# Optimization experiments

Hardware: AMD Instinct MI355X
Metric: run time of the kernel (lower is better)

The kernel has to match this reference:

```python
import jax, jax.numpy as jnp
import numpy as np
import math

B, L, H, E, D = 4, 1024, 8, 64, 64
T_STEPS = 1000


def setup_inputs() -> dict:
    key = jax.random.key(0)
    ks = jax.random.split(key, 6)
    queries = jax.random.normal(ks[0], (B, L, H, E), dtype=jnp.float32)
    keys = jax.random.normal(ks[1], (B, L, H, E), dtype=jnp.float32)
    values = jax.random.normal(ks[2], (B, L, H, D), dtype=jnp.float32)
    sigma = jax.random.normal(ks[3], (B, L, H), dtype=jnp.float32)
    sqrt_alphas_cumprod = jax.random.uniform(ks[4], (T_STEPS,), dtype=jnp.float32)
    t = jax.random.randint(ks[5], (B,), 0, T_STEPS)
    return {
        "queries": queries,
        "keys": keys,
        "values": values,
        "sigma": sigma,
        "sqrt_alphas_cumprod": sqrt_alphas_cumprod,
        "t": t,
    }


def reference(queries, keys, values, sigma, sqrt_alphas_cumprod, t):
    B_, L_, H_, E_ = queries.shape
    scale = 1.0 / math.sqrt(E_)

    # scores: [B,H,L,S]
    scores = jnp.einsum("blhe,bshe->bhls", queries, keys)
    # causal mask (triu, diagonal=1) -> -inf, then scale (mask_flag=True, attn_mask=None)
    causal = jnp.triu(jnp.ones((L_, L_), dtype=bool), k=1)
    attn = scale * jnp.where(causal, -jnp.inf, scores)

    # sigma pipeline: [B,L,H] -> [B,H,L] -> nonlinear chain
    sg = jnp.transpose(sigma, (0, 2, 1))               # [B,H,L]
    sg = jax.nn.sigmoid(sg * 5.0) + 1e-5
    sg = jnp.power(3.0, sg) - 1.0                      # in (0, 2)

    # per-batch diffusion scale: sqrt_alphas_cumprod[t] -> [B,1,1]
    sac_t = sqrt_alphas_cumprod[t][:, None, None]      # [B,1,1]
    sigma_t = jnp.broadcast_to((sac_t * sg)[..., None], (B_, H_, L_, L_))

    # |i-j| distance matrix, Gaussian prior
    idx = jnp.arange(L_)
    dist = jnp.abs(idx[:, None] - idx[None, :]).astype(jnp.float32)  # [L,L]
    inv_sqrt_2pi = 1.0 / math.sqrt(2.0 * math.pi)
    prior = inv_sqrt_2pi / sigma_t * jnp.exp(-(dist ** 2) / 2.0 / (sigma_t ** 2))

    series = jax.nn.softmax(attn, axis=-1)             # dropout p=0.0
    V = jnp.einsum("bhls,bshd->blhd", series, values)
    return V, series, prior, sigma_t
```

## Files before the change

### kernel.cpp

```cpp
#include <hip/hip_runtime.h>
#include <hip/hip_bf16.h>
#include <cstddef>
#include <cstdint>

namespace {

using f32x4  = __attribute__((ext_vector_type(4))) float;
using bf16x8 = __attribute__((ext_vector_type(8))) short;
using u16x2  = __attribute__((ext_vector_type(2))) unsigned short;
using u16x4  = __attribute__((ext_vector_type(4))) unsigned short;

constexpr int TOTAL_BLOCKS = 9216;
constexpr int PSTR = 1032;

__device__ inline unsigned short f2bf(float x) {
  __hip_bfloat16 hv = __float2bfloat16(x);
  return *reinterpret_cast<unsigned short*>(&hv);
}
__device__ inline float bf2f(unsigned short u) {
  return __uint_as_float(((unsigned int)u) << 16);
}
__device__ inline bf16x8 pack_bf8(f32x4 a, f32x4 b) {
  bf16x8 r;
  r[0] = (short)f2bf(a[0]); r[1] = (short)f2bf(a[1]);
  r[2] = (short)f2bf(a[2]); r[3] = (short)f2bf(a[3]);
  r[4] = (short)f2bf(b[0]); r[5] = (short)f2bf(b[1]);
  r[6] = (short)f2bf(b[2]); r[7] = (short)f2bf(b[3]);
  return r;
}

__global__ __launch_bounds__(256) void fused_all(
    const float* __restrict__ Qg, const float* __restrict__ Kg,
    const float* __restrict__ Vg, const float* __restrict__ Sg,
    const float* __restrict__ sacg, const int* __restrict__ tg,
    float* __restrict__ outV, float* __restrict__ outS,
    float* __restrict__ outP, float* __restrict__ outT)
{
  __shared__ unsigned short Pl[32 * PSTR];
  __shared__ unsigned short Vt[64 * 72];
  __shared__ float red[4][32];
  __shared__ float invl[32];

  const int tid = threadIdx.x;
  const int bid = blockIdx.x;
  const int role9 = bid / 9;

  if (bid - role9 * 9 != 0) {
    const int pb = role9 * 8 + (bid - role9 * 9) - 1;
    const int r0 = pb * 4 + (tid >> 6);
    const int ln = tid & 63;
    const int b  = r0 >> 13;
    const int hh = (r0 >> 10) & 7;
    const int l  = r0 & 1023;
    const float sgv = Sg[(size_t)(b * 1024 + l) * 8 + hh];
    const float sac = sacg[tg[b]];
    const float sig = 1.f / (1.f + __expf(-5.f * sgv)) + 1e-5f;
    const float st  = sac * expm1f(sig * 1.0986122886681098f);
    const float coef = 0.3989422804014327f / st;
    const float qc   = -0.5f / (st * st);
    float* pp = outP + ((size_t)r0 << 10);
    float* tp = outT + ((size_t)r0 << 10);
    const f32x4 stv = {st, st, st, st};
#pragma unroll
    for (int j = 0; j < 4; ++j) {
      const int c0 = j * 256 + ln * 4;
      const float d0 = (float)(l - c0);
      const float d1 = d0 - 1.f, d2 = d0 - 2.f, d3 = d0 - 3.f;
      f32x4 pr;
      pr[0] = coef * __expf(qc * d0 * d0);
      pr[1] = coef * __expf(qc * d1 * d1);
      pr[2] = coef * __expf(qc * d2 * d2);
      pr[3] = coef * __expf(qc * d3 * d3);
      __builtin_nontemporal_store(pr, reinterpret_cast<f32x4*>(pp + c0));
      __builtin_nontemporal_store(stv, reinterpret_cast<f32x4*>(tp + c0));
    }
    return;
  }

  const int aid = role9;
  const int w = tid >> 6, ln = tid & 63;
  const int g = ln >> 4, n16 = ln & 15;
  const int bh = aid & 31, b = bh >> 3, h = bh & 7;
  const int qt = 31 - (aid >> 5);
  const int qb = qt * 32;
  const int nch = (qt >> 1) + 1;

  const float* Qbase = Qg + ((size_t)(b * 1024) * 8 + h) * 64;
  const float* Kbase = Kg + ((size_t)(b * 1024) * 8 + h) * 64;
  const float* Vbase = Vg + ((size_t)(b * 1024) * 8 + h) * 64;

  bf16x8 qf[2][2];
#pragma unroll
  for (int u = 0; u < 2; ++u) {
    const float* qr = Qbase + (size_t)(qb + u * 16 + n16) * 512 + 8 * g;
    qf[u][0] = pack_bf8(*(const f32x4*)(qr),      *(const f32x4*)(qr + 4));
    qf[u][1] = pack_bf8(*(const f32x4*)(qr + 32), *(const f32x4*)(qr + 36));
  }

  f32x4 O[2] = {};
  float cs[2] = {0.f, 0.f};

  const int spair = tid & 31, dgrp = tid >> 5;

  for (int c = 0; c < nch; ++c) {
    const float* kr = Kbase + (size_t)(c * 64 + w * 16 + n16) * 512 + 8 * g;
    const bf16x8 kf0 = pack_bf8(*(const f32x4*)(kr),      *(const f32x4*)(kr + 4));
    const bf16x8 kf1 = pack_bf8(*(const f32x4*)(kr + 32), *(const f32x4*)(kr + 36));

    const float* vb = Vbase + (size_t)(c * 64 + 2 * spair) * 512 + dgrp * 8;
    const f32x4 va0 = *(const f32x4*)(vb);
    const f32x4 va1 = *(const f32x4*)(vb + 4);
    const f32x4 vc0 = *(const f32x4*)(vb + 512);
    const f32x4 vc1 = *(const f32x4*)(vb + 516);

    __syncthreads();

#pragma unroll
    for (int i = 0; i < 4; ++i) {
      u16x2 w0 = {f2bf(va0[i]), f2bf(vc0[i])};
      *reinterpret_cast<u16x2*>(&Vt[(dgrp * 8 + i) * 72 + 2 * spair]) = w0;
      u16x2 w1 = {f2bf(va1[i]), f2bf(vc1[i])};
      *reinterpret_cast<u16x2*>(&Vt[(dgrp * 8 + 4 + i) * 72 + 2 * spair]) = w1;
    }

#pragma unroll
    for (int u = 0; u < 2; ++u) {
      f32x4 acc = {0.f, 0.f, 0.f, 0.f};
      acc = __builtin_amdgcn_mfma_f32_16x16x32_bf16(kf0, qf[u][0], acc, 0, 0, 0);
      acc = __builtin_amdgcn_mfma_f32_16x16x32_bf16(kf1, qf[u][1], acc, 0, 0, 0);
      const int qlane = qb + u * 16 + n16;
      const int sbase = c * 64 + w * 16 + 4 * g;
      const float e0 = (sbase + 0 <= qlane) ? __expf(acc[0] * 0.125f) : 0.f;
      const float e1 = (sbase + 1 <= qlane) ? __expf(acc[1] * 0.125f) : 0.f;
      const float e2 = (sbase + 2 <= qlane) ? __expf(acc[2] * 0.125f) : 0.f;
      const float e3 = (sbase + 3 <= qlane) ? __expf(acc[3] * 0.125f) : 0.f;
      cs[u] += (e0 + e1) + (e2 + e3);
      u16x4 pk = {f2bf(e0), f2bf(e1), f2bf(e2), f2bf(e3)};
      *reinterpret_cast<u16x4*>(&Pl[(u * 16 + n16) * PSTR + sbase]) = pk;
    }

    __syncthreads();

#pragma unroll
    for (int u = 0; u < 2; ++u)
#pragma unroll
      for (int h2 = 0; h2 < 2; ++h2) {
        const bf16x8 pa =
            *reinterpret_cast<const bf16x8*>(&Pl[(u * 16 + n16) * PSTR + c * 64 + h2 * 32 + 8 * g]);
        const bf16x8 vv =
            *reinterpret_cast<const bf16x8*>(&Vt[(w * 16 + n16) * 72 + h2 * 32 + 8 * g]);
        O[u] = __builtin_amdgcn_mfma_f32_16x16x32_bf16(pa, vv, O[u], 0, 0, 0);
      }
  }

  cs[0] += __shfl_xor(cs[0], 16); cs[0] += __shfl_xor(cs[0], 32);
  cs[1] += __shfl_xor(cs[1], 16); cs[1] += __shfl_xor(cs[1], 32);
  if (ln < 16) { red[w][n16] = cs[0]; red[w][16 + n16] = cs[1]; }
  __syncthreads();
  if (tid < 32) {
    const float s = red[0][tid] + red[1][tid] + red[2][tid] + red[3][tid];
    invl[tid] = 1.f / s;
  }
  __syncthreads();

  {
    float* Vo = outV + ((size_t)(b * 1024) * 8 + h) * 64;
#pragma unroll
    for (int u = 0; u < 2; ++u)
#pragma unroll
      for (int r = 0; r < 4; ++r) {
        const int qrow = u * 16 + 4 * g + r;
        __builtin_nontemporal_store(O[u][r] * invl[qrow],
                                    Vo + (size_t)(qb + qrow) * 512 + w * 16 + n16);
      }
  }

  {
    const int r = tid >> 3, sub = tid & 7;
    float* Srow = outS + ((size_t)bh * 1024 + qb + r) * 1024;
    const float il = invl[r];
    const int slim = nch * 64;
#pragma unroll 4
    for (int j = 0; j < 32; ++j) {
      const int s = j * 32 + sub * 4;
      f32x4 o;
      if (s < slim) {
        const u16x4 p = *reinterpret_cast<const u16x4*>(&Pl[r * PSTR + s]);
        o[0] = bf2f(p[0]) * il;
        o[1] = bf2f(p[1]) * il;
        o[2] = bf2f(p[2]) * il;
        o[3] = bf2f(p[3]) * il;
      } else {
        o = (f32x4){0.f, 0.f, 0.f, 0.f};
      }
      __builtin_nontemporal_store(o, reinterpret_cast<f32x4*>(Srow + s));
    }
  }
}

}

extern "C" void kernel_launch(void* const* d_in, const int* in_sizes, int n_in,
                              void* d_out, int out_size, void* d_ws, size_t ws_size,
                              hipStream_t stream) {
  const float* Qg   = (const float*)d_in[0];
  const float* Kg   = (const float*)d_in[1];
  const float* Vg   = (const float*)d_in[2];
  const float* Sg   = (const float*)d_in[3];
  const float* sacg = (const float*)d_in[4];
  const int*   tg   = (const int*)d_in[5];

  float* out  = (float*)d_out;
  float* outV = out;
  float* outS = out + (size_t)2097152;
  float* outP = out + (size_t)35651584;
  float* outT = out + (size_t)69206016;

  hipLaunchKernelGGL(fused_all, dim3(TOTAL_BLOCKS), dim3(256), 0, stream,
                     Qg, Kg, Vg, Sg, sacg, tg, outV, outS, outP, outT);
}
```

Baseline: 82.50 us.

## Load V fragments directly into registers with double-buffered prefetch, drop LDS transpose

Removes the shared-memory staging and transpose of V, along with one barrier per chunk. Each lane now loads its MFMA B-operand V fragment straight from global memory as strided scalar loads. The next chunk's values are prefetched into a ping-pong register buffer while the current chunk is computed, to overlap global latency with compute. In exchange it issues 16 scalar strided loads per lane instead of 4 vector loads, and uses more registers.

```diff
diff --git a/kernel.cpp b/kernel.cpp
--- a/kernel.cpp
+++ b/kernel.cpp
@@ -7,7 +7,6 @@
 
 using f32x4  = __attribute__((ext_vector_type(4))) float;
 using bf16x8 = __attribute__((ext_vector_type(8))) short;
-using u16x2  = __attribute__((ext_vector_type(2))) unsigned short;
 using u16x4  = __attribute__((ext_vector_type(4))) unsigned short;
 
 constexpr int TOTAL_BLOCKS = 9216;
@@ -26,6 +25,12 @@
   r[2] = (short)f2bf(a[2]); r[3] = (short)f2bf(a[3]);
   r[4] = (short)f2bf(b[0]); r[5] = (short)f2bf(b[1]);
   r[6] = (short)f2bf(b[2]); r[7] = (short)f2bf(b[3]);
+  return r;
+}
+__device__ inline bf16x8 pack8(const float* p) {
+  bf16x8 r;
+#pragma unroll
+  for (int i = 0; i < 8; ++i) r[i] = (short)f2bf(p[i]);
   return r;
 }
 
@@ -37,7 +42,6 @@
     float* __restrict__ outP, float* __restrict__ outT)
 {
   __shared__ unsigned short Pl[32 * PSTR];
-  __shared__ unsigned short Vt[64 * 72];
   __shared__ float red[4][32];
   __shared__ float invl[32];
 
@@ -100,28 +104,22 @@
   f32x4 O[2] = {};
   float cs[2] = {0.f, 0.f};
 
-  const int spair = tid & 31, dgrp = tid >> 5;
-
-  for (int c = 0; c < nch; ++c) {
+  const float* vcol = Vbase + (size_t)(8 * g) * 512 + w * 16 + n16;
+
+  float vrA[16], vrB[16];
+  auto vload = [&](int c, float (&dst)[16]) {
+    const float* p = vcol + (size_t)c * 64 * 512;
+#pragma unroll
+    for (int h2 = 0; h2 < 2; ++h2)
+#pragma unroll
+      for (int j = 0; j < 8; ++j)
+        dst[h2 * 8 + j] = p[(size_t)(32 * h2 + j) * 512];
+  };
+
+  auto body = [&](int c, float (&vc)[16], float (&vn)[16]) {
     const float* kr = Kbase + (size_t)(c * 64 + w * 16 + n16) * 512 + 8 * g;
     const bf16x8 kf0 = pack_bf8(*(const f32x4*)(kr),      *(const f32x4*)(kr + 4));
     const bf16x8 kf1 = pack_bf8(*(const f32x4*)(kr + 32), *(const f32x4*)(kr + 36));
-
-    const float* vb = Vbase + (size_t)(c * 64 + 2 * spair) * 512 + dgrp * 8;
-    const f32x4 va0 = *(const f32x4*)(vb);
-    const f32x4 va1 = *(const f32x4*)(vb + 4);
-    const f32x4 vc0 = *(const f32x4*)(vb + 512);
-    const f32x4 vc1 = *(const f32x4*)(vb + 516);
-
-    __syncthreads();
-
-#pragma unroll
-    for (int i = 0; i < 4; ++i) {
-      u16x2 w0 = {f2bf(va0[i]), f2bf(vc0[i])};
-      *reinterpret_cast<u16x2*>(&Vt[(dgrp * 8 + i) * 72 + 2 * spair]) = w0;
-      u16x2 w1 = {f2bf(va1[i]), f2bf(vc1[i])};
-      *reinterpret_cast<u16x2*>(&Vt[(dgrp * 8 + 4 + i) * 72 + 2 * spair]) = w1;
-    }
 
 #pragma unroll
     for (int u = 0; u < 2; ++u) {
@@ -139,18 +137,30 @@
       *reinterpret_cast<u16x4*>(&Pl[(u * 16 + n16) * PSTR + sbase]) = pk;
     }
 
+    if (c + 1 < nch) vload(c + 1, vn);
+
     __syncthreads();
 
-#pragma unroll
-    for (int u = 0; u < 2; ++u)
-#pragma unroll
-      for (int h2 = 0; h2 < 2; ++h2) {
-        const bf16x8 pa =
-            *reinterpret_cast<const bf16x8*>(&Pl[(u * 16 + n16) * PSTR + c * 64 + h2 * 32 + 8 * g]);
-        const bf16x8 vv =
-            *reinterpret_cast<const bf16x8*>(&Vt[(w * 16 + n16) * 72 + h2 * 32 + 8 * g]);
-        O[u] = __builtin_amdgcn_mfma_f32_16x16x32_bf16(pa, vv, O[u], 0, 0, 0);
-      }
+    const bf16x8 vv0 = pack8(&vc[0]);
+    const bf16x8 vv1 = pack8(&vc[8]);
+#pragma unroll
+    for (int u = 0; u < 2; ++u) {
+      const bf16x8 pa0 =
+          *reinterpret_cast<const bf16x8*>(&Pl[(u * 16 + n16) * PSTR + c * 64 + 8 * g]);
+      O[u] = __builtin_amdgcn_mfma_f32_16x16x32_bf16(pa0, vv0, O[u], 0, 0, 0);
+      const bf16x8 pa1 =
+          *reinterpret_cast<const bf16x8*>(&Pl[(u * 16 + n16) * PSTR + c * 64 + 32 + 8 * g]);
+      O[u] = __builtin_amdgcn_mfma_f32_16x16x32_bf16(pa1, vv1, O[u], 0, 0, 0);
+    }
+  };
+
+  vload(0, vrA);
+  int c = 0;
+  while (true) {
+    body(c, vrA, vrB);
+    if (++c >= nch) break;
+    body(c, vrB, vrA);
+    if (++c >= nch) break;
   }
 
   cs[0] += __shfl_xor(cs[0], 16); cs[0] += __shfl_xor(cs[0], 32);
```

Measured after the change: 81.46 us. About the same (-1.3%).
